# Kernel optimization log

Measured on AMD Instinct MI355X. Metric: run time of the kernel, lower is better.

Reference implementation:

```python
import jax, jax.numpy as jnp
import numpy as np

N = 50000      # nodes
E = 800000     # edges (avg degree 16)
IN = 256       # in_size
HID = 64       # hid_size
H = 4          # n_head
OUT = 64       # out_size


def setup_inputs() -> dict:
    key = jax.random.key(0)
    ks = jax.random.split(key, 16)
    g = lambda k, shp: jax.random.normal(k, shp, jnp.float32) * 0.1
    return {
        "features": jax.random.normal(ks[0], (N, IN), jnp.float32),
        "src": jax.random.randint(ks[1], (E,), 0, N, jnp.int32),
        "dst": jax.random.randint(ks[2], (E,), 0, N, jnp.int32),
        # layer 0: 256 -> 4 heads x 64
        "W0": g(ks[3], (IN, H * HID)), "al0": g(ks[4], (H, HID)), "ar0": g(ks[5], (H, HID)), "b0": g(ks[6], (H * HID,)),
        # layer 1: 256 -> 4 heads x 64
        "W1": g(ks[7], (H * HID, H * HID)), "al1": g(ks[8], (H, HID)), "ar1": g(ks[9], (H, HID)), "b1": g(ks[10], (H * HID,)),
        # layer 2: 256 -> 4 heads x 64, relu activation, mean over heads
        "W2": g(ks[11], (H * HID, H * OUT)), "al2": g(ks[12], (H, OUT)), "ar2": g(ks[13], (H, OUT)), "b2": g(ks[14], (H * OUT,)),
    }


def gat_conv(h, src, dst, W, al, ar, b, apply_relu):
    """DGL GATConv (eval mode, dropout off), residual identity since in == H*D."""
    n = h.shape[0]
    hh, dd = al.shape
    feat = (h @ W).reshape(n, hh, dd)                       # [N,H,D]
    el = jnp.einsum('nhd,hd->nh', feat, al)                 # [N,H]
    er = jnp.einsum('nhd,hd->nh', feat, ar)                 # [N,H]
    e = jax.nn.leaky_relu(el[src] + er[dst], negative_slope=0.2)  # [E,H]
    # segment softmax over incoming edges of each dst node
    m = jax.ops.segment_max(e, dst, num_segments=n)         # [N,H]
    ex = jnp.exp(e - m[dst])
    den = jax.ops.segment_sum(ex, dst, num_segments=n)      # [N,H]
    alpha = ex / den[dst]                                   # [E,H]
    rst = jax.ops.segment_sum(feat[src] * alpha[..., None], dst, num_segments=n)  # [N,H,D]
    rst = rst + h.reshape(n, hh, dd) + b.reshape(1, hh, dd)  # residual + bias
    return jax.nn.relu(rst) if apply_relu else rst


def reference(features, src, dst, W0, al0, ar0, b0, W1, al1, ar1, b1, W2, al2, ar2, b2):
    h = gat_conv(features, src, dst, W0, al0, ar0, b0, False).reshape(N, -1)
    h = gat_conv(h, src, dst, W1, al1, ar1, b1, False).reshape(N, -1)
    h = gat_conv(h, src, dst, W2, al2, ar2, b2, True).mean(axis=1)  # [N,OUT]
    return h
```

## Files before the change

kernel.cpp:

```cpp
#include <hip/hip_runtime.h>

#define NNODE 50000
#define NEDGE 800000
#define NH 4
#define DH 64
#define HD 256
#define PADN 50048
#define EPAD 64

typedef __attribute__((ext_vector_type(8))) short short8v;
typedef __attribute__((ext_vector_type(4))) float float4v;
typedef __attribute__((ext_vector_type(4))) unsigned short ushort4v;

static __device__ __forceinline__ float b2f(unsigned short u) {
  union { float f; unsigned v; } x; x.v = ((unsigned)u) << 16; return x.f;
}
static __device__ __forceinline__ unsigned short f2b(float f) {
  unsigned u = __builtin_bit_cast(unsigned, f);
  u += 0x7fff + ((u >> 16) & 1);
  return (unsigned short)(u >> 16);
}

__global__ __launch_bounds__(256) void k_cvt(const float* __restrict__ in,
                                             unsigned short* __restrict__ outb) {
  int i = (blockIdx.x * 256 + threadIdx.x) * 4;
  float4v v = *(const float4v*)(in + i);
  ushort4v o;
  o.x = f2b(v.x); o.y = f2b(v.y); o.z = f2b(v.z); o.w = f2b(v.w);
  *(ushort4v*)(outb + i) = o;
}

__global__ __launch_bounds__(256) void k_cvtw(const float* __restrict__ W0,
                                              const float* __restrict__ W1,
                                              const float* __restrict__ W2,
                                              unsigned short* __restrict__ T0,
                                              unsigned short* __restrict__ T1,
                                              unsigned short* __restrict__ T2) {
  const float* W = blockIdx.y == 0 ? W0 : (blockIdx.y == 1 ? W1 : W2);
  unsigned short* T = blockIdx.y == 0 ? T0 : (blockIdx.y == 1 ? T1 : T2);
  int k = blockIdx.x;
  int nn = threadIdx.x;
  T[nn * HD + k] = f2b(W[k * HD + nn]);
}

__global__ void k_edge(const int* __restrict__ src, const int* __restrict__ dst,
                       int* __restrict__ fill, int* __restrict__ csrp) {
  int e = blockIdx.x * 256 + threadIdx.x;
  if (e < NEDGE) {
    int d = dst[e];
    int pos = atomicAdd(&fill[d], 1);
    if (pos < EPAD) csrp[(d << 6) + pos] = src[e];
  }
}

__global__ __launch_bounds__(256) void k_gemm(const unsigned short* __restrict__ Ab,
                                              const unsigned short* __restrict__ Wt,
                                              const float* __restrict__ al,
                                              const float* __restrict__ ar,
                                              unsigned short* __restrict__ featb,
                                              float* __restrict__ el,
                                              float* __restrict__ er) {
  __shared__ unsigned short As[8][64][32];
  const int row0 = blockIdx.x * 64;
  const int tid = threadIdx.x;
  const int lane = tid & 63;
  const int head = tid >> 6;
  const int lr = lane & 15;
  const int kf = (lane >> 4) * 8;

  const unsigned short* gsrc = Ab + (size_t)(row0 + (tid >> 2)) * HD + (tid & 3) * 8;

#define STAGE(t)                                                                        \
  __builtin_amdgcn_global_load_lds(                                                     \
      (const __attribute__((address_space(1))) unsigned int*)(gsrc + (t) * 32),         \
      (__attribute__((address_space(3))) unsigned int*)&As[t][tid >> 2][(tid & 3) * 8], \
      16, 0, 0)

  float4v acc[4][4] = {};

#pragma unroll
  for (int t = 0; t < 8; ++t) STAGE(t);
  __syncthreads();
#undef STAGE

#pragma unroll
  for (int t = 0; t < 8; ++t) {
    short8v af[4], bfr[4];
#pragma unroll
    for (int ni = 0; ni < 4; ++ni)
      bfr[ni] = *(const short8v*)(Wt + (size_t)(head * 64 + ni * 16 + lr) * HD + t * 32 + kf);
#pragma unroll
    for (int mi = 0; mi < 4; ++mi)
      af[mi] = *(const short8v*)&As[t][mi * 16 + lr][kf];
#pragma unroll
    for (int mi = 0; mi < 4; ++mi)
#pragma unroll
      for (int ni = 0; ni < 4; ++ni)
        acc[mi][ni] = __builtin_amdgcn_mfma_f32_16x16x32_bf16(af[mi], bfr[ni], acc[mi][ni], 0, 0, 0);
  }

  float alv[4], arv[4];
#pragma unroll
  for (int ni = 0; ni < 4; ++ni) {
    alv[ni] = al[head * 64 + ni * 16 + lr];
    arv[ni] = ar[head * 64 + ni * 16 + lr];
  }
  const int rg = (lane >> 4) * 4;
#pragma unroll
  for (int mi = 0; mi < 4; ++mi) {
#pragma unroll
    for (int reg = 0; reg < 4; ++reg) {
      int grow = row0 + mi * 16 + rg + reg;
      bool valid = grow < NNODE;
      float e1 = 0.f, e2 = 0.f;
#pragma unroll
      for (int ni = 0; ni < 4; ++ni) {
        float v = acc[mi][ni][reg];
        e1 = fmaf(v, alv[ni], e1);
        e2 = fmaf(v, arv[ni], e2);
        if (valid) featb[(size_t)grow * HD + head * 64 + ni * 16 + lr] = f2b(v);
      }
#pragma unroll
      for (int off = 1; off < 16; off <<= 1) {
        e1 += __shfl_xor(e1, off, 64);
        e2 += __shfl_xor(e2, off, 64);
      }
      if (lr == 0 && valid) {
        el[grow * NH + head] = e1;
        er[grow * NH + head] = e2;
      }
    }
  }
}

template <int LAYER>
__global__ __launch_bounds__(256) void k_agg(const int* __restrict__ fillarr,
                                             const int* __restrict__ csrp,
                                             const float* __restrict__ el,
                                             const float* __restrict__ er,
                                             const unsigned short* __restrict__ featb,
                                             const unsigned short* __restrict__ hinb,
                                             const float* __restrict__ bias,
                                             void* __restrict__ outv) {
  const int tid = threadIdx.x;
  const int w = tid >> 6;
  const int lane = tid & 63;
  const int n = blockIdx.x * 4 + w;
  const int e2 = lane >> 5;
  const int h = (lane >> 3) & 3;
  const int dg = lane & 7;
  const int deg = min(fillarr[n], EPAD);

  __shared__ float alpha_s[4][64][4];
  __shared__ int src_s[4][64];

  const float4v er4 = *(const float4v*)(er + n * 4);

  int s = 0;
  float4v lg = {-1e30f, -1e30f, -1e30f, -1e30f};
  if (lane < deg) {
    s = csrp[(n << 6) + lane];
    float4v e4 = *(const float4v*)(el + s * 4);
#pragma unroll
    for (int c = 0; c < 4; ++c) {
      float x = e4[c] + er4[c];
      lg[c] = x > 0.f ? x : 0.2f * x;
    }
  }
  float4v p;
#pragma unroll
  for (int c = 0; c < 4; ++c) p[c] = __expf(lg[c]);
  *(float4v*)&alpha_s[w][lane][0] = p;
  src_s[w][lane] = s;

  float4v denp = p;
#pragma unroll
  for (int off = 32; off; off >>= 1)
#pragma unroll
    for (int c = 0; c < 4; ++c) denp[c] += __shfl_xor(denp[c], off, 64);

  float acc[8] = {};
  const int foff = (h << 6) + (dg << 3);
  int nit = (((deg + 1) >> 1) + 3) & ~3;
  for (int pj = 0; pj < nit; pj += 4) {
    float a[4];
    int sv[4];
    uint4 u[4];
#pragma unroll
    for (int q = 0; q < 4; ++q) {
      int e = ((pj + q) << 1) + e2;
      a[q] = alpha_s[w][e][h];
      sv[q] = src_s[w][e];
    }
#pragma unroll
    for (int q = 0; q < 4; ++q)
      u[q] = *(const uint4*)(featb + ((size_t)sv[q] << 8) + foff);
#pragma unroll
    for (int q = 0; q < 4; ++q) {
      unsigned uu[4] = {u[q].x, u[q].y, u[q].z, u[q].w};
#pragma unroll
      for (int t = 0; t < 4; ++t) {
        float flo = __builtin_bit_cast(float, uu[t] << 16);
        float fhi = __builtin_bit_cast(float, uu[t] & 0xffff0000u);
        acc[2 * t] = fmaf(a[q], flo, acc[2 * t]);
        acc[2 * t + 1] = fmaf(a[q], fhi, acc[2 * t + 1]);
      }
    }
  }
#pragma unroll
  for (int k = 0; k < 8; ++k) acc[k] += __shfl_xor(acc[k], 32, 64);

  float dh = h == 0 ? denp[0] : (h == 1 ? denp[1] : (h == 2 ? denp[2] : denp[3]));
  float inv = dh > 0.f ? 1.f / dh : 0.f;

  uint4 hv = *(const uint4*)(hinb + ((size_t)n << 8) + foff);
  unsigned hh[4] = {hv.x, hv.y, hv.z, hv.w};
  const float4v* bp = (const float4v*)(bias + foff);
  float4v bb0 = bp[0], bb1 = bp[1];
  float bb[8] = {bb0.x, bb0.y, bb0.z, bb0.w, bb1.x, bb1.y, bb1.z, bb1.w};
  float v[8];
#pragma unroll
  for (int k = 0; k < 8; ++k) {
    unsigned hu = (k & 1) ? (hh[k >> 1] & 0xffff0000u) : (hh[k >> 1] << 16);
    v[k] = acc[k] * inv + __builtin_bit_cast(float, hu) + bb[k];
  }

  if (LAYER == 2) {
#pragma unroll
    for (int k = 0; k < 8; ++k) {
      v[k] = fmaxf(v[k], 0.f);
      v[k] += __shfl_xor(v[k], 8, 64);
      v[k] += __shfl_xor(v[k], 16, 64);
      v[k] *= 0.25f;
    }
    if (lane < 8) {
      float* out = (float*)outv + (size_t)n * DH + (dg << 3);
      *(float4v*)out = (float4v){v[0], v[1], v[2], v[3]};
      *(float4v*)(out + 4) = (float4v){v[4], v[5], v[6], v[7]};
    }
  } else {
    if (e2 == 0) {
      uint4 o;
      unsigned ov[4];
#pragma unroll
      for (int q = 0; q < 4; ++q)
        ov[q] = (unsigned)f2b(v[2 * q]) | ((unsigned)f2b(v[2 * q + 1]) << 16);
      o.x = ov[0]; o.y = ov[1]; o.z = ov[2]; o.w = ov[3];
      *(uint4*)((unsigned short*)outv + ((size_t)n << 8) + foff) = o;
    }
  }
}

extern "C" void kernel_launch(void* const* d_in, const int* in_sizes, int n_in,
                              void* d_out, int out_size, void* d_ws, size_t ws_size,
                              hipStream_t stream) {
  const float* features = (const float*)d_in[0];
  const int* src = (const int*)d_in[1];
  const int* dst = (const int*)d_in[2];
  const float* W0 = (const float*)d_in[3];
  const float* al0 = (const float*)d_in[4];
  const float* ar0 = (const float*)d_in[5];
  const float* b0 = (const float*)d_in[6];
  const float* W1 = (const float*)d_in[7];
  const float* al1 = (const float*)d_in[8];
  const float* ar1 = (const float*)d_in[9];
  const float* b1 = (const float*)d_in[10];
  const float* W2 = (const float*)d_in[11];
  const float* al2 = (const float*)d_in[12];
  const float* ar2 = (const float*)d_in[13];
  const float* b2 = (const float*)d_in[14];
  float* out = (float*)d_out;

  char* p = (char*)d_ws;
  auto carve = [&](size_t bytes) {
    char* q = p;
    p += (bytes + 255) & ~(size_t)255;
    return q;
  };
  unsigned short* h0b = (unsigned short*)carve((size_t)PADN * HD * 2);
  unsigned short* h1b = (unsigned short*)carve((size_t)PADN * HD * 2);
  unsigned short* featb = (unsigned short*)carve((size_t)PADN * HD * 2);
  unsigned short* wt0 = (unsigned short*)carve((size_t)HD * HD * 2);
  unsigned short* wt1 = (unsigned short*)carve((size_t)HD * HD * 2);
  unsigned short* wt2 = (unsigned short*)carve((size_t)HD * HD * 2);
  float* el = (float*)carve((size_t)NNODE * NH * 4);
  float* er = (float*)carve((size_t)NNODE * NH * 4);
  int* fill = (int*)carve((size_t)NNODE * 4);
  int* csrp = (int*)carve((size_t)NNODE * EPAD * 4);
  unsigned short* h2b = h0b;

  hipMemsetAsync(fill, 0, (size_t)NNODE * 4, stream);
  hipMemsetAsync(csrp, 0, (size_t)NNODE * EPAD * 4, stream);

  k_cvt<<<NNODE * HD / (256 * 4), 256, 0, stream>>>(features, h0b);
  k_cvtw<<<dim3(HD, 3), 256, 0, stream>>>(W0, W1, W2, wt0, wt1, wt2);
  k_edge<<<NEDGE / 256, 256, 0, stream>>>(src, dst, fill, csrp);

  dim3 gg(PADN / 64);

  k_gemm<<<gg, 256, 0, stream>>>(h0b, wt0, al0, ar0, featb, el, er);
  k_agg<0><<<NNODE / 4, 256, 0, stream>>>(fill, csrp, el, er, featb, h0b, b0, h1b);

  k_gemm<<<gg, 256, 0, stream>>>(h1b, wt1, al1, ar1, featb, el, er);
  k_agg<1><<<NNODE / 4, 256, 0, stream>>>(fill, csrp, el, er, featb, h1b, b1, h2b);

  k_gemm<<<gg, 256, 0, stream>>>(h2b, wt2, al2, ar2, featb, el, er);
  k_agg<2><<<NNODE / 4, 256, 0, stream>>>(fill, csrp, el, er, featb, h2b, b2, (void*)out);
}
```

Before: 359.7 us.

## Fold attention vectors into weights, stage GEMM output via LDS, deepen gather

```diff
diff --git a/kernel.cpp b/kernel.cpp
--- a/kernel.cpp
+++ b/kernel.cpp
@@ -43,6 +43,39 @@
   T[nn * HD + k] = f2b(W[k * HD + nn]);
 }
 
+__global__ __launch_bounds__(256) void k_wal(const float* __restrict__ W0,
+                                             const float* __restrict__ W1,
+                                             const float* __restrict__ W2,
+                                             const float* __restrict__ al0,
+                                             const float* __restrict__ ar0,
+                                             const float* __restrict__ al1,
+                                             const float* __restrict__ ar1,
+                                             const float* __restrict__ al2,
+                                             const float* __restrict__ ar2,
+                                             unsigned short* __restrict__ T0,
+                                             unsigned short* __restrict__ T1,
+                                             unsigned short* __restrict__ T2) {
+  int L = blockIdx.y;
+  const float* W = L == 0 ? W0 : (L == 1 ? W1 : W2);
+  const float* al = L == 0 ? al0 : (L == 1 ? al1 : al2);
+  const float* ar = L == 0 ? ar0 : (L == 1 ? ar1 : ar2);
+  unsigned short* T = L == 0 ? T0 : (L == 1 ? T1 : T2);
+  int k = threadIdx.x;
+  const float* wr = W + k * HD;
+  float s[8] = {};
+#pragma unroll 4
+  for (int h = 0; h < 4; ++h)
+    for (int d = 0; d < 64; ++d) {
+      float wv = wr[h * 64 + d];
+      s[h] = fmaf(wv, al[h * 64 + d], s[h]);
+      s[4 + h] = fmaf(wv, ar[h * 64 + d], s[4 + h]);
+    }
+#pragma unroll
+  for (int j = 0; j < 8; ++j) T[j * HD + k] = f2b(s[j]);
+#pragma unroll
+  for (int j = 8; j < 16; ++j) T[j * HD + k] = 0;
+}
+
 __global__ void k_edge(const int* __restrict__ src, const int* __restrict__ dst,
                        int* __restrict__ fill, int* __restrict__ csrp) {
   int e = blockIdx.x * 256 + threadIdx.x;
@@ -55,8 +88,7 @@
 
 __global__ __launch_bounds__(256) void k_gemm(const unsigned short* __restrict__ Ab,
                                               const unsigned short* __restrict__ Wt,
-                                              const float* __restrict__ al,
-                                              const float* __restrict__ ar,
+                                              const unsigned short* __restrict__ walr,
                                               unsigned short* __restrict__ featb,
                                               float* __restrict__ el,
                                               float* __restrict__ er) {
@@ -77,6 +109,7 @@
       16, 0, 0)
 
   float4v acc[4][4] = {};
+  float4v acc_e = {};
 
 #pragma unroll
   for (int t = 0; t < 8; ++t) STAGE(t);
@@ -85,10 +118,11 @@
 
 #pragma unroll
   for (int t = 0; t < 8; ++t) {
-    short8v af[4], bfr[4];
+    short8v af[4], bfr[4], bfe;
 #pragma unroll
     for (int ni = 0; ni < 4; ++ni)
       bfr[ni] = *(const short8v*)(Wt + (size_t)(head * 64 + ni * 16 + lr) * HD + t * 32 + kf);
+    bfe = *(const short8v*)(walr + (size_t)lr * HD + t * 32 + kf);
 #pragma unroll
     for (int mi = 0; mi < 4; ++mi)
       af[mi] = *(const short8v*)&As[t][mi * 16 + lr][kf];
@@ -97,39 +131,39 @@
 #pragma unroll
       for (int ni = 0; ni < 4; ++ni)
         acc[mi][ni] = __builtin_amdgcn_mfma_f32_16x16x32_bf16(af[mi], bfr[ni], acc[mi][ni], 0, 0, 0);
-  }
-
-  float alv[4], arv[4];
-#pragma unroll
-  for (int ni = 0; ni < 4; ++ni) {
-    alv[ni] = al[head * 64 + ni * 16 + lr];
-    arv[ni] = ar[head * 64 + ni * 16 + lr];
-  }
+    acc_e = __builtin_amdgcn_mfma_f32_16x16x32_bf16(af[head], bfe, acc_e, 0, 0, 0);
+  }
+
   const int rg = (lane >> 4) * 4;
-#pragma unroll
-  for (int mi = 0; mi < 4; ++mi) {
-#pragma unroll
-    for (int reg = 0; reg < 4; ++reg) {
-      int grow = row0 + mi * 16 + rg + reg;
-      bool valid = grow < NNODE;
-      float e1 = 0.f, e2 = 0.f;
-#pragma unroll
-      for (int ni = 0; ni < 4; ++ni) {
-        float v = acc[mi][ni][reg];
-        e1 = fmaf(v, alv[ni], e1);
-        e2 = fmaf(v, arv[ni], e2);
-        if (valid) featb[(size_t)grow * HD + head * 64 + ni * 16 + lr] = f2b(v);
-      }
-#pragma unroll
-      for (int off = 1; off < 16; off <<= 1) {
-        e1 += __shfl_xor(e1, off, 64);
-        e2 += __shfl_xor(e2, off, 64);
-      }
-      if (lr == 0 && valid) {
-        el[grow * NH + head] = e1;
-        er[grow * NH + head] = e2;
-      }
-    }
+  __syncthreads();
+  unsigned short* T = (unsigned short*)As;
+
+#pragma unroll
+  for (int mi = 0; mi < 4; ++mi)
+#pragma unroll
+    for (int ni = 0; ni < 4; ++ni)
+#pragma unroll
+      for (int reg = 0; reg < 4; ++reg)
+        T[(mi * 16 + rg + reg) * HD + head * 64 + ni * 16 + lr] = f2b(acc[mi][ni][reg]);
+
+#pragma unroll
+  for (int reg = 0; reg < 4; ++reg) {
+    int grow = row0 + head * 16 + rg + reg;
+    if (grow < NNODE) {
+      if (lr < 4) el[grow * NH + lr] = acc_e[reg];
+      else if (lr < 8) er[grow * NH + lr - 4] = acc_e[reg];
+    }
+  }
+
+  __syncthreads();
+#pragma unroll
+  for (int j = 0; j < 8; ++j) {
+    int seg = j * 256 + tid;
+    int row = seg >> 5, c16 = seg & 31;
+    int grow = row0 + row;
+    if (grow < NNODE)
+      *(uint4*)(featb + (size_t)grow * HD + c16 * 8) =
+          *(const uint4*)(T + row * HD + c16 * 8);
   }
 }
 
@@ -181,22 +215,22 @@
 
   float acc[8] = {};
   const int foff = (h << 6) + (dg << 3);
-  int nit = (((deg + 1) >> 1) + 3) & ~3;
-  for (int pj = 0; pj < nit; pj += 4) {
-    float a[4];
-    int sv[4];
-    uint4 u[4];
-#pragma unroll
-    for (int q = 0; q < 4; ++q) {
+  int nit = (((deg + 1) >> 1) + 7) & ~7;
+  for (int pj = 0; pj < nit; pj += 8) {
+    float a[8];
+    int sv[8];
+    uint4 u[8];
+#pragma unroll
+    for (int q = 0; q < 8; ++q) {
       int e = ((pj + q) << 1) + e2;
       a[q] = alpha_s[w][e][h];
       sv[q] = src_s[w][e];
     }
 #pragma unroll
-    for (int q = 0; q < 4; ++q)
+    for (int q = 0; q < 8; ++q)
       u[q] = *(const uint4*)(featb + ((size_t)sv[q] << 8) + foff);
 #pragma unroll
-    for (int q = 0; q < 4; ++q) {
+    for (int q = 0; q < 8; ++q) {
       unsigned uu[4] = {u[q].x, u[q].y, u[q].z, u[q].w};
 #pragma unroll
       for (int t = 0; t < 4; ++t) {
@@ -283,6 +317,9 @@
   unsigned short* wt0 = (unsigned short*)carve((size_t)HD * HD * 2);
   unsigned short* wt1 = (unsigned short*)carve((size_t)HD * HD * 2);
   unsigned short* wt2 = (unsigned short*)carve((size_t)HD * HD * 2);
+  unsigned short* wal0 = (unsigned short*)carve((size_t)16 * HD * 2);
+  unsigned short* wal1 = (unsigned short*)carve((size_t)16 * HD * 2);
+  unsigned short* wal2 = (unsigned short*)carve((size_t)16 * HD * 2);
   float* el = (float*)carve((size_t)NNODE * NH * 4);
   float* er = (float*)carve((size_t)NNODE * NH * 4);
   int* fill = (int*)carve((size_t)NNODE * 4);
@@ -290,20 +327,21 @@
   unsigned short* h2b = h0b;
 
   hipMemsetAsync(fill, 0, (size_t)NNODE * 4, stream);
-  hipMemsetAsync(csrp, 0, (size_t)NNODE * EPAD * 4, stream);
 
   k_cvt<<<NNODE * HD / (256 * 4), 256, 0, stream>>>(features, h0b);
   k_cvtw<<<dim3(HD, 3), 256, 0, stream>>>(W0, W1, W2, wt0, wt1, wt2);
+  k_wal<<<dim3(1, 3), 256, 0, stream>>>(W0, W1, W2, al0, ar0, al1, ar1, al2, ar2,
+                                        wal0, wal1, wal2);
   k_edge<<<NEDGE / 256, 256, 0, stream>>>(src, dst, fill, csrp);
 
   dim3 gg(PADN / 64);
 
-  k_gemm<<<gg, 256, 0, stream>>>(h0b, wt0, al0, ar0, featb, el, er);
+  k_gemm<<<gg, 256, 0, stream>>>(h0b, wt0, wal0, featb, el, er);
   k_agg<0><<<NNODE / 4, 256, 0, stream>>>(fill, csrp, el, er, featb, h0b, b0, h1b);
 
-  k_gemm<<<gg, 256, 0, stream>>>(h1b, wt1, al1, ar1, featb, el, er);
+  k_gemm<<<gg, 256, 0, stream>>>(h1b, wt1, wal1, featb, el, er);
   k_agg<1><<<NNODE / 4, 256, 0, stream>>>(fill, csrp, el, er, featb, h1b, b1, h2b);
 
-  k_gemm<<<gg, 256, 0, stream>>>(h2b, wt2, al2, ar2, featb, el, er);
+  k_gemm<<<gg, 256, 0, stream>>>(h2b, wt2, wal2, featb, el, er);
   k_agg<2><<<NNODE / 4, 256, 0, stream>>>(fill, csrp, el, er, featb, h2b, b2, (void*)out);
 }
```

Result: slower. 464.6 us (+29.2%).
